# Performance work log

Hardware: AMD Instinct MI355X
Metric: run time of the kernel (lower is better)

Reference implementation:

```python
import jax, jax.numpy as jnp
import numpy as np
import math

B, T, D = 2, 2048, 1024
H, HS = 16, 64  # n_heads, head_size; D == H*HS


def setup_inputs() -> dict:
    key = jax.random.key(0)
    k1, k2, k3 = jax.random.split(key, 3)
    x = jax.random.normal(k1, (B, T, D), dtype=jnp.float32)
    w_qkv = jax.random.normal(k2, (D, 3 * D), dtype=jnp.float32) * (1.0 / math.sqrt(D))
    b_qkv = jnp.zeros((3 * D,), dtype=jnp.float32)
    w_out = jax.random.normal(k3, (D, D), dtype=jnp.float32) * (1.0 / math.sqrt(D))
    b_out = jnp.zeros((D,), dtype=jnp.float32)
    return {"x": x, "w_qkv": w_qkv, "b_qkv": b_qkv, "w_out": w_out, "b_out": b_out}


def reference(x, w_qkv, b_qkv, w_out, b_out):
    b, t, d = x.shape
    qkv = x @ w_qkv + b_qkv                       # (B,T,3D)
    q, k, v = jnp.split(qkv, 3, axis=-1)
    # (B,T,D) -> (B,H,T,HS)
    q = q.reshape(b, t, H, HS).transpose(0, 2, 1, 3)
    k = k.reshape(b, t, H, HS).transpose(0, 2, 1, 3)
    v = v.reshape(b, t, H, HS).transpose(0, 2, 1, 3)
    scale = 1.0 / math.sqrt(HS)
    attn = jnp.einsum('bhqd,bhkd->bhqk', q, k) * scale  # (B,H,T,T)
    causal = jnp.tril(jnp.ones((t, t), dtype=bool))
    attn = jnp.where(causal[None, None], attn, -jnp.inf)
    attn = jax.nn.softmax(attn, axis=-1)
    o = jnp.einsum('bhqk,bhkd->bhqd', attn, v)          # (B,H,T,HS)
    o = o.transpose(0, 2, 1, 3).reshape(b, t, d)
    return o @ w_out + b_out
```

## Files before the change

### kernel.cpp

```cpp
#include <hip/hip_runtime.h>
#include <math.h>

#define B_  2
#define T_  2048
#define D_  1024
#define H_  16
#define HS_ 64
#define M_  (B_*T_)

typedef __bf16 bf16x8 __attribute__((ext_vector_type(8)));
typedef float  f32x4  __attribute__((ext_vector_type(4)));
typedef unsigned short u16;

static __device__ __forceinline__ u16 f2bf(float f) {
    unsigned int u = __float_as_uint(f);
    u += 0x7fff + ((u >> 16) & 1);
    return (u16)(u >> 16);
}

static __device__ __forceinline__ void glds16(const u16* g, u16* l) {
    __builtin_amdgcn_global_load_lds(
        (const __attribute__((address_space(1))) void*)g,
        (__attribute__((address_space(3))) void*)l, 16, 0, 0);
}

static __device__ __forceinline__ bf16x8 lds_chunk4(const u16* base, int row, int c) {
    return *reinterpret_cast<const bf16x8*>(base + (size_t)(row * 4 + (c ^ ((row >> 1) & 3))) * 8);
}

static __device__ __forceinline__ bf16x8 lds_chunk(const u16* base, int row, int c) {
    return *reinterpret_cast<const bf16x8*>(base + (size_t)(row * 8 + (c ^ (row & 7))) * 8);
}

__global__ __launch_bounds__(256) void prep_kernel(
    const float* __restrict__ x, const float* __restrict__ w_qkv,
    const float* __restrict__ w_out,
    u16* __restrict__ Xb, u16* __restrict__ WqkvT, u16* __restrict__ WoutT)
{
    int bid = blockIdx.x;
    if (bid < 4096) {
        int i = (bid * 256 + threadIdx.x) * 4;
        float4 v = *reinterpret_cast<const float4*>(x + i);
        ushort4 o;
        o.x = f2bf(v.x); o.y = f2bf(v.y); o.z = f2bf(v.z); o.w = f2bf(v.w);
        *reinterpret_cast<ushort4*>(Xb + i) = o;
        return;
    }
    const float* in; u16* out; int C; int c0, r0;
    if (bid < 4096 + 3072) {
        int t = bid - 4096;
        in = w_qkv; out = WqkvT; C = 3 * D_;
        c0 = (t % 96) * 32; r0 = (t / 96) * 32;
    } else {
        int t = bid - 7168;
        in = w_out; out = WoutT; C = D_;
        c0 = (t & 31) * 32; r0 = (t >> 5) * 32;
    }
    __shared__ float tile[32][33];
    int tr = threadIdx.x >> 3, tc4 = (threadIdx.x & 7) * 4;
    float4 v = *reinterpret_cast<const float4*>(in + (size_t)(r0 + tr) * C + c0 + tc4);
    tile[tr][tc4+0] = v.x; tile[tr][tc4+1] = v.y;
    tile[tr][tc4+2] = v.z; tile[tr][tc4+3] = v.w;
    __syncthreads();
    ushort4 o;
    o.x = f2bf(tile[tc4+0][tr]); o.y = f2bf(tile[tc4+1][tr]);
    o.z = f2bf(tile[tc4+2][tr]); o.w = f2bf(tile[tc4+3][tr]);
    *reinterpret_cast<ushort4*>(out + (size_t)(c0 + tr) * D_ + r0 + tc4) = o;
}

template<int MODE>
__global__ __launch_bounds__(256) void gemm_bt(
    const u16* __restrict__ A, const u16* __restrict__ Bt,
    const float* __restrict__ bias,
    float* __restrict__ Cf,
    u16* __restrict__ Qb, u16* __restrict__ Kb, u16* __restrict__ Vt,
    int M, int N, int K)
{
    __shared__ u16 As[128 * 32];
    __shared__ u16 Bs[128 * 32];
    int tid  = threadIdx.x;
    int lane = tid & 63, wave = tid >> 6;
    int wm = wave >> 1, wn = wave & 1;
    int quad = lane >> 4, lr = lane & 15;
    int bm = blockIdx.x, bn = blockIdx.y;

    f32x4 acc[4][4] = {};

    const u16* Ab = A  + (size_t)(bm * 128) * K;
    const u16* Bb = Bt + (size_t)(bn * 128) * K;

    int r0 = tid >> 2,         c0 = (((tid) & 3) ^ ((tid >> 3) & 3)) * 8;
    int r1 = (tid + 256) >> 2, c1 = (((tid + 256) & 3) ^ (((tid + 256) >> 3) & 3)) * 8;

    for (int k0 = 0; k0 < K; k0 += 32) {
        __syncthreads();
        glds16(Ab + (size_t)r0 * K + k0 + c0, As + (size_t)tid * 8);
        glds16(Ab + (size_t)r1 * K + k0 + c1, As + (size_t)(tid + 256) * 8);
        glds16(Bb + (size_t)r0 * K + k0 + c0, Bs + (size_t)tid * 8);
        glds16(Bb + (size_t)r1 * K + k0 + c1, Bs + (size_t)(tid + 256) * 8);
        __syncthreads();
        bf16x8 af[4], bfr[4];
        #pragma unroll
        for (int i = 0; i < 4; ++i)
            af[i] = lds_chunk4(As, wm*64 + i*16 + lr, quad);
        #pragma unroll
        for (int j = 0; j < 4; ++j)
            bfr[j] = lds_chunk4(Bs, wn*64 + j*16 + lr, quad);
        #pragma unroll
        for (int i = 0; i < 4; ++i)
            #pragma unroll
            for (int j = 0; j < 4; ++j)
                acc[i][j] = __builtin_amdgcn_mfma_f32_16x16x32_bf16(af[i], bfr[j], acc[i][j], 0, 0, 0);
    }

    #pragma unroll
    for (int i = 0; i < 4; ++i) {
        int mrow = bm*128 + wm*64 + i*16 + quad*4;
        #pragma unroll
        for (int j = 0; j < 4; ++j) {
            int ncol = bn*128 + wn*64 + j*16 + lr;
            float bv = bias[ncol];
            #pragma unroll
            for (int r = 0; r < 4; ++r) {
                float v = acc[i][j][r] + bv;
                int m = mrow + r;
                if (MODE == 1) {
                    Cf[(size_t)m * N + ncol] = v;
                } else {
                    int b = m >> 11, t = m & (T_ - 1);
                    int s = ncol >> 10, rem = ncol & 1023;
                    int h = rem >> 6, d = rem & 63;
                    int bh = b * H_ + h;
                    if (s == 0)      Qb[((size_t)bh*T_ + t)*HS_ + d] = f2bf(v * 0.125f);
                    else if (s == 1) Kb[((size_t)bh*T_ + t)*HS_ + d] = f2bf(v);
                    else             Vt[((size_t)bh*HS_ + d)*T_ + t] = f2bf(v);
                }
            }
        }
    }
}

__global__ __launch_bounds__(256) void attn_kernel(
    const u16* __restrict__ Qb, const u16* __restrict__ Kb,
    const u16* __restrict__ Vt, u16* __restrict__ Ob)
{
    __shared__ u16 Ks[64 * 64];
    __shared__ u16 Vs[64 * 64];
    __shared__ u16 Ps[4][32 * 64];

    int tid  = threadIdx.x;
    int lane = tid & 63, wave = tid >> 6;
    int quad = lane >> 4, lr = lane & 15;

    int lin = blockIdx.x;
    int bh  = (lin & 7) + 8 * ((lin >> 3) & 3);
    int p   = lin >> 5;

    int grp  = wave >> 1;
    int wg   = wave & 1;
    int myst = grp ? (31 - p) : p;
    int qb   = myst * 64 + wg * 32;
    int jd   = myst;
    int jmax = 31 - p;

    bf16x8 qf[2][2];
    #pragma unroll
    for (int mi = 0; mi < 2; ++mi)
        #pragma unroll
        for (int h2 = 0; h2 < 2; ++h2)
            qf[mi][h2] = *reinterpret_cast<const bf16x8*>(
                Qb + ((size_t)bh*T_ + qb + mi*16 + lr)*HS_ + h2*32 + quad*8);

    f32x4 Oa[2][4] = {};
    float lrow[2][4] = {};

    int srow = tid >> 3;
    int scol = ((tid & 7) ^ (srow & 7)) * 8;
    const u16* Kst0 = Kb + ((size_t)bh*T_ + srow     )*HS_ + scol;
    const u16* Kst1 = Kb + ((size_t)bh*T_ + srow + 32)*HS_ + scol;
    const u16* Vst0 = Vt + ((size_t)bh*HS_ + srow     )*T_ + scol;
    const u16* Vst1 = Vt + ((size_t)bh*HS_ + srow + 32)*T_ + scol;

    bf16x8 kpre0 = *reinterpret_cast<const bf16x8*>(Kst0);
    bf16x8 kpre1 = *reinterpret_cast<const bf16x8*>(Kst1);
    bf16x8 vpre0 = *reinterpret_cast<const bf16x8*>(Vst0);
    bf16x8 vpre1 = *reinterpret_cast<const bf16x8*>(Vst1);

    for (int jt = 0; jt <= jmax; ++jt) {
        __syncthreads();
        reinterpret_cast<bf16x8*>(Ks)[tid]       = kpre0;
        reinterpret_cast<bf16x8*>(Ks)[tid + 256] = kpre1;
        reinterpret_cast<bf16x8*>(Vs)[tid]       = vpre0;
        reinterpret_cast<bf16x8*>(Vs)[tid + 256] = vpre1;
        if (jt < jmax) {
            size_t kn = (size_t)(jt + 1) * 64;
            kpre0 = *reinterpret_cast<const bf16x8*>(Kst0 + kn * HS_);
            kpre1 = *reinterpret_cast<const bf16x8*>(Kst1 + kn * HS_);
            vpre0 = *reinterpret_cast<const bf16x8*>(Vst0 + kn);
            vpre1 = *reinterpret_cast<const bf16x8*>(Vst1 + kn);
        }
        __syncthreads();

        if (jt <= jd) {
            int kb = jt * 64;
            f32x4 Sa[2][4] = {};
            #pragma unroll
            for (int kk = 0; kk < 2; ++kk) {
                int c = kk * 4 + quad;
                #pragma unroll
                for (int nt = 0; nt < 4; ++nt) {
                    bf16x8 bk = lds_chunk(Ks, nt*16 + lr, c);
                    #pragma unroll
                    for (int mi = 0; mi < 2; ++mi)
                        Sa[mi][nt] = __builtin_amdgcn_mfma_f32_16x16x32_bf16(
                            qf[mi][kk], bk, Sa[mi][nt], 0, 0, 0);
                }
            }

            if (jt == jd) {
                #pragma unroll
                for (int mi = 0; mi < 2; ++mi)
                    #pragma unroll
                    for (int nt = 0; nt < 4; ++nt)
                        #pragma unroll
                        for (int r = 0; r < 4; ++r) {
                            int kg = kb + nt*16 + lr;
                            int qg = qb + mi*16 + quad*4 + r;
                            if (kg > qg) Sa[mi][nt][r] = -INFINITY;
                        }
            }

            #pragma unroll
            for (int mi = 0; mi < 2; ++mi)
                #pragma unroll
                for (int nt = 0; nt < 4; ++nt)
                    #pragma unroll
                    for (int r = 0; r < 4; ++r) {
                        float pv = __expf(Sa[mi][nt][r]);
                        lrow[mi][r] += pv;
                        int prow = mi*16 + quad*4 + r;
                        int c = nt*2 + (lr >> 3);
                        Ps[wave][(size_t)(prow*8 + (c ^ (prow & 7)))*8 + (lr & 7)] = f2bf(pv);
                    }

            #pragma unroll
            for (int kk = 0; kk < 2; ++kk) {
                int c = kk * 4 + quad;
                bf16x8 pa[2];
                #pragma unroll
                for (int mi = 0; mi < 2; ++mi)
                    pa[mi] = lds_chunk(Ps[wave], mi*16 + lr, c);
                #pragma unroll
                for (int nt = 0; nt < 4; ++nt) {
                    bf16x8 vb = lds_chunk(Vs, nt*16 + lr, c);
                    #pragma unroll
                    for (int mi = 0; mi < 2; ++mi)
                        Oa[mi][nt] = __builtin_amdgcn_mfma_f32_16x16x32_bf16(
                            pa[mi], vb, Oa[mi][nt], 0, 0, 0);
                }
            }
        }
    }

    int b = bh >> 4, h = bh & 15;
    #pragma unroll
    for (int mi = 0; mi < 2; ++mi)
        #pragma unroll
        for (int r = 0; r < 4; ++r) {
            float s = lrow[mi][r];
            #pragma unroll
            for (int off = 8; off >= 1; off >>= 1)
                s += __shfl_xor(s, off, 64);
            float inv = 1.f / s;
            int qg = qb + mi*16 + quad*4 + r;
            #pragma unroll
            for (int nt = 0; nt < 4; ++nt) {
                int d = nt*16 + lr;
                Ob[((size_t)b*T_ + qg)*D_ + h*HS_ + d] = f2bf(Oa[mi][nt][r] * inv);
            }
        }
}

extern "C" void kernel_launch(void* const* d_in, const int* in_sizes, int n_in,
                              void* d_out, int out_size, void* d_ws, size_t ws_size,
                              hipStream_t stream) {
    (void)in_sizes; (void)n_in; (void)out_size; (void)ws_size;
    const float* x     = (const float*)d_in[0];
    const float* w_qkv = (const float*)d_in[1];
    const float* b_qkv = (const float*)d_in[2];
    const float* w_out = (const float*)d_in[3];
    const float* b_out = (const float*)d_in[4];
    float* out = (float*)d_out;

    char* ws = (char*)d_ws;
    u16* Xb    = (u16*)ws; ws += (size_t)M_ * D_ * 2;
    u16* WqkvT = (u16*)ws; ws += (size_t)3 * D_ * D_ * 2;
    u16* WoutT = (u16*)ws; ws += (size_t)D_ * D_ * 2;
    u16* Qb    = (u16*)ws; ws += (size_t)M_ * D_ * 2;
    u16* Kb    = (u16*)ws; ws += (size_t)M_ * D_ * 2;
    u16* Vt    = (u16*)ws; ws += (size_t)M_ * D_ * 2;
    u16* Ob    = (u16*)ws; ws += (size_t)M_ * D_ * 2;

    prep_kernel<<<8192, 256, 0, stream>>>(x, w_qkv, w_out, Xb, WqkvT, WoutT);
    gemm_bt<0><<<dim3(M_/128, 3*D_/128), 256, 0, stream>>>(
        Xb, WqkvT, b_qkv, nullptr, Qb, Kb, Vt, M_, 3*D_, D_);
    attn_kernel<<<512, 256, 0, stream>>>(Qb, Kb, Vt, Ob);
    gemm_bt<1><<<dim3(M_/128, D_/128), 256, 0, stream>>>(
        Ob, WoutT, b_out, out, nullptr, nullptr, nullptr, M_, D_, D_);
}
```

Baseline: 206.4 us.

## Split attention into one query tile per block and vectorize V-transpose stores

The attention kernel no longer pairs two query tiles (early and late) per block with two waves each. Each block now handles a single 64-row query tile, one 16-row slice per wave, and the grid doubles to 1024 blocks with a snake ordering of tiles for load balance. This cuts per-wave registers and LDS and raises parallelism, but K/V tiles are loaded once per query tile instead of being shared by two tiles. The QKV GEMM epilogue also packs four consecutive t values into one ushort4 store for the transposed V layout instead of four scalar stores.

```diff
diff --git a/kernel.cpp b/kernel.cpp
--- a/kernel.cpp
+++ b/kernel.cpp
@@ -115,25 +115,36 @@
 
     #pragma unroll
     for (int i = 0; i < 4; ++i) {
-        int mrow = bm*128 + wm*64 + i*16 + quad*4;
+        int m0 = bm*128 + wm*64 + i*16 + quad*4;
         #pragma unroll
         for (int j = 0; j < 4; ++j) {
             int ncol = bn*128 + wn*64 + j*16 + lr;
             float bv = bias[ncol];
-            #pragma unroll
-            for (int r = 0; r < 4; ++r) {
-                float v = acc[i][j][r] + bv;
-                int m = mrow + r;
-                if (MODE == 1) {
-                    Cf[(size_t)m * N + ncol] = v;
+            float v4[4];
+            #pragma unroll
+            for (int r = 0; r < 4; ++r) v4[r] = acc[i][j][r] + bv;
+            if (MODE == 1) {
+                #pragma unroll
+                for (int r = 0; r < 4; ++r)
+                    Cf[(size_t)(m0 + r) * N + ncol] = v4[r];
+            } else {
+                int b = m0 >> 11, t0 = m0 & (T_ - 1);
+                int s = ncol >> 10, rem = ncol & 1023;
+                int h = rem >> 6, d = rem & 63;
+                int bh = b * H_ + h;
+                if (s == 0) {
+                    #pragma unroll
+                    for (int r = 0; r < 4; ++r)
+                        Qb[((size_t)bh*T_ + t0 + r)*HS_ + d] = f2bf(v4[r] * 0.125f);
+                } else if (s == 1) {
+                    #pragma unroll
+                    for (int r = 0; r < 4; ++r)
+                        Kb[((size_t)bh*T_ + t0 + r)*HS_ + d] = f2bf(v4[r]);
                 } else {
-                    int b = m >> 11, t = m & (T_ - 1);
-                    int s = ncol >> 10, rem = ncol & 1023;
-                    int h = rem >> 6, d = rem & 63;
-                    int bh = b * H_ + h;
-                    if (s == 0)      Qb[((size_t)bh*T_ + t)*HS_ + d] = f2bf(v * 0.125f);
-                    else if (s == 1) Kb[((size_t)bh*T_ + t)*HS_ + d] = f2bf(v);
-                    else             Vt[((size_t)bh*HS_ + d)*T_ + t] = f2bf(v);
+                    ushort4 o;
+                    o.x = f2bf(v4[0]); o.y = f2bf(v4[1]);
+                    o.z = f2bf(v4[2]); o.w = f2bf(v4[3]);
+                    *reinterpret_cast<ushort4*>(&Vt[((size_t)bh*HS_ + d)*T_ + t0]) = o;
                 }
             }
         }
@@ -146,7 +157,7 @@
 {
     __shared__ u16 Ks[64 * 64];
     __shared__ u16 Vs[64 * 64];
-    __shared__ u16 Ps[4][32 * 64];
+    __shared__ u16 Ps[4][16 * 64];
 
     int tid  = threadIdx.x;
     int lane = tid & 63, wave = tid >> 6;
@@ -154,25 +165,18 @@
 
     int lin = blockIdx.x;
     int bh  = (lin & 7) + 8 * ((lin >> 3) & 3);
-    int p   = lin >> 5;
-
-    int grp  = wave >> 1;
-    int wg   = wave & 1;
-    int myst = grp ? (31 - p) : p;
-    int qb   = myst * 64 + wg * 32;
-    int jd   = myst;
-    int jmax = 31 - p;
-
-    bf16x8 qf[2][2];
+    int idx = lin >> 5;
+    int qt  = idx < 16 ? idx : 47 - idx;
+    int qw  = qt * 64 + wave * 16;
+
+    const u16* Qp = Qb + ((size_t)bh * T_ + qw) * HS_;
+    bf16x8 qf[2];
     #pragma unroll
-    for (int mi = 0; mi < 2; ++mi)
-        #pragma unroll
-        for (int h2 = 0; h2 < 2; ++h2)
-            qf[mi][h2] = *reinterpret_cast<const bf16x8*>(
-                Qb + ((size_t)bh*T_ + qb + mi*16 + lr)*HS_ + h2*32 + quad*8);
-
-    f32x4 Oa[2][4] = {};
-    float lrow[2][4] = {};
+    for (int h2 = 0; h2 < 2; ++h2)
+        qf[h2] = *reinterpret_cast<const bf16x8*>(Qp + lr*HS_ + h2*32 + quad*8);
+
+    f32x4 Oa[4] = {};
+    float lrow[4] = {0.f, 0.f, 0.f, 0.f};
 
     int srow = tid >> 3;
     int scol = ((tid & 7) ^ (srow & 7)) * 8;
@@ -186,13 +190,13 @@
     bf16x8 vpre0 = *reinterpret_cast<const bf16x8*>(Vst0);
     bf16x8 vpre1 = *reinterpret_cast<const bf16x8*>(Vst1);
 
-    for (int jt = 0; jt <= jmax; ++jt) {
+    for (int jt = 0; jt <= qt; ++jt) {
         __syncthreads();
         reinterpret_cast<bf16x8*>(Ks)[tid]       = kpre0;
         reinterpret_cast<bf16x8*>(Ks)[tid + 256] = kpre1;
         reinterpret_cast<bf16x8*>(Vs)[tid]       = vpre0;
         reinterpret_cast<bf16x8*>(Vs)[tid + 256] = vpre1;
-        if (jt < jmax) {
+        if (jt < qt) {
             size_t kn = (size_t)(jt + 1) * 64;
             kpre0 = *reinterpret_cast<const bf16x8*>(Kst0 + kn * HS_);
             kpre1 = *reinterpret_cast<const bf16x8*>(Kst1 + kn * HS_);
@@ -201,84 +205,67 @@
         }
         __syncthreads();
 
-        if (jt <= jd) {
-            int kb = jt * 64;
-            f32x4 Sa[2][4] = {};
-            #pragma unroll
-            for (int kk = 0; kk < 2; ++kk) {
-                int c = kk * 4 + quad;
+        int kb = jt * 64;
+        f32x4 Sa[4] = {};
+        #pragma unroll
+        for (int kk = 0; kk < 2; ++kk) {
+            int c = kk * 4 + quad;
+            #pragma unroll
+            for (int nt = 0; nt < 4; ++nt) {
+                bf16x8 bk = lds_chunk(Ks, nt*16 + lr, c);
+                Sa[nt] = __builtin_amdgcn_mfma_f32_16x16x32_bf16(qf[kk], bk, Sa[nt], 0, 0, 0);
+            }
+        }
+
+        if (jt == qt) {
+            #pragma unroll
+            for (int nt = 0; nt < 4; ++nt)
                 #pragma unroll
-                for (int nt = 0; nt < 4; ++nt) {
-                    bf16x8 bk = lds_chunk(Ks, nt*16 + lr, c);
-                    #pragma unroll
-                    for (int mi = 0; mi < 2; ++mi)
-                        Sa[mi][nt] = __builtin_amdgcn_mfma_f32_16x16x32_bf16(
-                            qf[mi][kk], bk, Sa[mi][nt], 0, 0, 0);
+                for (int r = 0; r < 4; ++r) {
+                    int kg = kb + nt*16 + lr;
+                    int qg = qw + quad*4 + r;
+                    if (kg > qg) Sa[nt][r] = -INFINITY;
                 }
-            }
-
-            if (jt == jd) {
-                #pragma unroll
-                for (int mi = 0; mi < 2; ++mi)
-                    #pragma unroll
-                    for (int nt = 0; nt < 4; ++nt)
-                        #pragma unroll
-                        for (int r = 0; r < 4; ++r) {
-                            int kg = kb + nt*16 + lr;
-                            int qg = qb + mi*16 + quad*4 + r;
-                            if (kg > qg) Sa[mi][nt][r] = -INFINITY;
-                        }
-            }
-
-            #pragma unroll
-            for (int mi = 0; mi < 2; ++mi)
-                #pragma unroll
-                for (int nt = 0; nt < 4; ++nt)
-                    #pragma unroll
-                    for (int r = 0; r < 4; ++r) {
-                        float pv = __expf(Sa[mi][nt][r]);
-                        lrow[mi][r] += pv;
-                        int prow = mi*16 + quad*4 + r;
-                        int c = nt*2 + (lr >> 3);
-                        Ps[wave][(size_t)(prow*8 + (c ^ (prow & 7)))*8 + (lr & 7)] = f2bf(pv);
-                    }
-
-            #pragma unroll
-            for (int kk = 0; kk < 2; ++kk) {
-                int c = kk * 4 + quad;
-                bf16x8 pa[2];
-                #pragma unroll
-                for (int mi = 0; mi < 2; ++mi)
-                    pa[mi] = lds_chunk(Ps[wave], mi*16 + lr, c);
-                #pragma unroll
-                for (int nt = 0; nt < 4; ++nt) {
-                    bf16x8 vb = lds_chunk(Vs, nt*16 + lr, c);
-                    #pragma unroll
-                    for (int mi = 0; mi < 2; ++mi)
-                        Oa[mi][nt] = __builtin_amdgcn_mfma_f32_16x16x32_bf16(
-                            pa[mi], vb, Oa[mi][nt], 0, 0, 0);
-                }
+        }
+
+        #pragma unroll
+        for (int nt = 0; nt < 4; ++nt)
+            #pragma unroll
+            for (int r = 0; r < 4; ++r) {
+                float pv = __expf(Sa[nt][r]);
+                lrow[r] += pv;
+                int prow = quad*4 + r;
+                int c = nt*2 + (lr >> 3);
+                Ps[wave][(size_t)(prow*8 + (c ^ (prow & 7)))*8 + (lr & 7)] = f2bf(pv);
+            }
+
+        #pragma unroll
+        for (int kk = 0; kk < 2; ++kk) {
+            int c = kk * 4 + quad;
+            bf16x8 pa = lds_chunk(Ps[wave], lr, c);
+            #pragma unroll
+            for (int nt = 0; nt < 4; ++nt) {
+                bf16x8 vb = lds_chunk(Vs, nt*16 + lr, c);
+                Oa[nt] = __builtin_amdgcn_mfma_f32_16x16x32_bf16(pa, vb, Oa[nt], 0, 0, 0);
             }
         }
     }
 
     int b = bh >> 4, h = bh & 15;
     #pragma unroll
-    for (int mi = 0; mi < 2; ++mi)
-        #pragma unroll
-        for (int r = 0; r < 4; ++r) {
-            float s = lrow[mi][r];
-            #pragma unroll
-            for (int off = 8; off >= 1; off >>= 1)
-                s += __shfl_xor(s, off, 64);
-            float inv = 1.f / s;
-            int qg = qb + mi*16 + quad*4 + r;
-            #pragma unroll
-            for (int nt = 0; nt < 4; ++nt) {
-                int d = nt*16 + lr;
-                Ob[((size_t)b*T_ + qg)*D_ + h*HS_ + d] = f2bf(Oa[mi][nt][r] * inv);
-            }
-        }
+    for (int r = 0; r < 4; ++r) {
+        float s = lrow[r];
+        #pragma unroll
+        for (int off = 8; off >= 1; off >>= 1)
+            s += __shfl_xor(s, off, 64);
+        float inv = 1.f / s;
+        int qg = qw + quad*4 + r;
+        #pragma unroll
+        for (int nt = 0; nt < 4; ++nt) {
+            int d = nt*16 + lr;
+            Ob[((size_t)b*T_ + qg)*D_ + h*HS_ + d] = f2bf(Oa[nt][r] * inv);
+        }
+    }
 }
 
 extern "C" void kernel_launch(void* const* d_in, const int* in_sizes, int n_in,
@@ -304,7 +291,7 @@
     prep_kernel<<<8192, 256, 0, stream>>>(x, w_qkv, w_out, Xb, WqkvT, WoutT);
     gemm_bt<0><<<dim3(M_/128, 3*D_/128), 256, 0, stream>>>(
         Xb, WqkvT, b_qkv, nullptr, Qb, Kb, Vt, M_, 3*D_, D_);
-    attn_kernel<<<512, 256, 0, stream>>>(Qb, Kb, Vt, Ob);
+    attn_kernel<<<1024, 256, 0, stream>>>(Qb, Kb, Vt, Ob);
     gemm_bt<1><<<dim3(M_/128, D_/128), 256, 0, stream>>>(
         Ob, WoutT, b_out, out, nullptr, nullptr, nullptr, M_, D_, D_);
 }
```

New measurement: 185.6 us. 10.0% less time.
